# Kernel tuning notes

Measured on AMD Instinct MI355X. Metric: run time of the kernel, lower is better.

Reference implementation:

```python
import jax, jax.numpy as jnp
import numpy as np

P = 3          # graph partitions
CO = 64        # out_channels
KS = 9         # temporal kernel size (Gamma)
STRIDE = 1     # temporal stride
EPS = 1e-3     # keras BatchNormalization default epsilon


def setup_inputs() -> dict:
    key = jax.random.key(0)
    k1, k2, k3 = jax.random.split(key, 3)
    x = jax.random.normal(k1, (32, 64, 300, 25), dtype=jnp.float32)      # (N, C_in, L, V)
    A = jax.random.uniform(k2, (3, 25, 25), dtype=jnp.float32)           # (P, V, V)
    W = jax.random.normal(k3, (64, 192), dtype=jnp.float32) * 0.05       # (C_in, C_out*P)
    gamma = jnp.ones((64,), dtype=jnp.float32)
    beta = jnp.zeros((64,), dtype=jnp.float32)
    mean = jnp.zeros((64,), dtype=jnp.float32)
    var = jnp.ones((64,), dtype=jnp.float32)
    return {"x": x, "A": A, "W": W, "gamma": gamma, "beta": beta, "mean": mean, "var": var}


def _lt_matrix(L):
    # sum of shifted identities: lt[r, r + i*STRIDE] = 1 for i in [0, KS//STRIDE)
    lt = jnp.zeros((L, L), dtype=jnp.float32)
    for i in range(KS // STRIDE):
        lt = lt + jnp.eye(L, k=i * STRIDE, dtype=jnp.float32)
    return lt


def reference(x, A, W, gamma, beta, mean, var):
    N, C, L, V = x.shape
    res = x  # identity residual (in_channels == out_channels, stride == 1)
    # 1x1 conv: (N,C,L,V) x (C, CO*P) -> (N, CO*P, L, V); channel k = c*P + p (split into CO groups of P)
    y = jnp.einsum('nclv,ck->nklv', x, W)
    y = y.reshape(N, CO, P, L, V)  # (N, C_out, P, L, V)
    # partitioned graph matmul over joints: contract V with A[p]
    z = jnp.einsum('ncplv,pvw->ncplw', y, A)
    # temporal aggregation via handcrafted banded matrix, then sum over partitions
    lt = _lt_matrix(L)
    t = jnp.einsum('ncplv,lm->ncmv', z, lt)  # partition sum fused into einsum
    # BN (inference) over channel axis + ReLU
    inv = gamma / jnp.sqrt(var + EPS)
    xn = (t - mean[None, :, None, None]) * inv[None, :, None, None] + beta[None, :, None, None]
    xn = jax.nn.relu(xn)
    # residual add + final ReLU (dropout is identity at inference)
    return jax.nn.relu(xn + res)
```

## Files before the change

### kernel.cpp

```cpp
#include <hip/hip_runtime.h>
#include <cstdint>
#include <cstddef>

typedef short bf16x8 __attribute__((ext_vector_type(8)));
typedef float f32x4 __attribute__((ext_vector_type(4)));

#define EPS 1e-3f

__device__ __forceinline__ short f32_to_bf16s(float f) {
    union { float f; uint32_t u; } v; v.f = f;
    return (short)((v.u + 0x7FFFu + ((v.u >> 16) & 1u)) >> 16);
}

__global__ __launch_bounds__(256) void prep_kernel(const float* __restrict__ A,
                                                   const float* __restrict__ W,
                                                   unsigned short* __restrict__ wt,
                                                   unsigned short* __restrict__ at) {
    int idx = blockIdx.x * 256 + threadIdx.x;
    if (idx < 12288) {
        int kp = idx >> 6, ci = idx & 63;
        wt[idx] = (unsigned short)f32_to_bf16s(W[ci * 192 + kp]);
    } else {
        int j = idx - 12288;
        if (j < 3072) {
            int w = j / 96, k = j - w * 96;
            float val = 0.f;
            if (w < 25 && k < 75) {
                int p = k / 25, v = k - p * 25;
                val = A[(p * 25 + v) * 25 + w];
            }
            at[j] = (unsigned short)f32_to_bf16s(val);
        }
    }
}

__global__ __launch_bounds__(512, 4) void mega_kernel(
    const float* __restrict__ x,
    const unsigned short* __restrict__ wt,
    const unsigned short* __restrict__ at,
    const float* __restrict__ gamma, const float* __restrict__ beta,
    const float* __restrict__ mean, const float* __restrict__ var,
    float* __restrict__ out) {
    const int lin = blockIdx.x + 38 * blockIdx.y;
    const int logical = (lin & 7) * 152 + (lin >> 3);
    const int ch = logical % 38;
    const int n  = logical / 38;

    const int l0 = ch * 8;
    const int tid = threadIdx.x;
    const int wv = tid >> 6, lane = tid & 63, q = lane >> 4, lcol = lane & 15;

    __shared__ __align__(16) short smem[13312];
    __shared__ float scs[64], shs[64];

    bf16x8 b2[2][3];
    #pragma unroll
    for (int nt = 0; nt < 2; ++nt)
        #pragma unroll
        for (int s = 0; s < 3; ++s)
            b2[nt][s] = *(const bf16x8*)(at + (size_t)(nt * 16 + lcol) * 96 + 32 * s + 8 * q);
    if (tid < 64) {
        float sc = gamma[tid] * rsqrtf(var[tid] + EPS);
        scs[tid] = sc;
        shs[tid] = beta[tid] - mean[tid] * sc;
    }

    #pragma unroll 1
    for (int rep = 0; rep < 4; ++rep) {
        int cidx = tid + rep * 512;
        if (cidx < 1600) {
            int ci = cidx / 25, v = cidx - ci * 25;
            const float* xp = x + (size_t)(n * 64 + ci) * 7500 + v;
            float vals[16];
            #pragma unroll
            for (int i = 0; i < 16; ++i) {
                int l = l0 - 8 + i;
                vals[i] = (l >= 0 && l < 300) ? xp[l * 25] : 0.f;
            }
            float run = vals[0] + vals[1] + vals[2] + vals[3]
                      + vals[4] + vals[5] + vals[6] + vals[7];
            short* wb = &smem[(ci >> 3) * 1656 + (ci & 7)];
            #pragma unroll
            for (int j = 0; j < 8; ++j) {
                run += vals[j + 8];
                wb[(j * 25 + v) * 8] = f32_to_bf16s(run);
                run -= vals[j];
            }
        }
    }
    __syncthreads();

    bf16x8 b1[2][2];
    #pragma unroll
    for (int nt = 0; nt < 2; ++nt) {
        int col = wv * 25 + nt * 16 + lcol;
        #pragma unroll
        for (int s = 0; s < 2; ++s)
            b1[nt][s] = *(const bf16x8*)&smem[(4 * s + q) * 1656 + col * 8];
    }
    __syncthreads();

    #pragma unroll
    for (int i = lane; i < 512; i += 64) {
        int r = i >> 5, cc = 72 + (i & 31);
        smem[(wv * 16 + r) * 104 + cc] = 0;
    }

    const int lg = l0 + wv;
    const size_t outrow = ((size_t)n * 64 * 300 + lg) * 25;

    #pragma unroll 1
    for (int g = 0; g < 4; ++g) {
        bf16x8 a1[3][2];
        #pragma unroll
        for (int mt = 0; mt < 3; ++mt)
            #pragma unroll
            for (int s = 0; s < 2; ++s)
                a1[mt][s] = *(const bf16x8*)(wt + (size_t)(g * 48 + mt * 16 + lcol) * 64 + 32 * s + 8 * q);

        f32x4 acc[3][2];
        #pragma unroll
        for (int mt = 0; mt < 3; ++mt)
            #pragma unroll
            for (int nt = 0; nt < 2; ++nt) acc[mt][nt] = (f32x4){0.f, 0.f, 0.f, 0.f};
        #pragma unroll
        for (int s = 0; s < 2; ++s)
            #pragma unroll
            for (int mt = 0; mt < 3; ++mt) {
                bf16x8 av = a1[mt][s];
                #pragma unroll
                for (int nt = 0; nt < 2; ++nt)
                    acc[mt][nt] = __builtin_amdgcn_mfma_f32_16x16x32_bf16(av, b1[nt][s], acc[mt][nt], 0, 0, 0);
            }

        float res[2][4];
        #pragma unroll
        for (int nt = 0; nt < 2; ++nt) {
            int w = nt * 16 + lcol;
            bool val = (w < 25) && (lg < 300);
            #pragma unroll
            for (int r = 0; r < 4; ++r) {
                int c = g * 16 + 4 * q + r;
                res[nt][r] = val ? x[outrow + (size_t)c * 7500 + w] : 0.f;
            }
        }

        #pragma unroll
        for (int mt = 0; mt < 3; ++mt)
            #pragma unroll
            for (int nt = 0; nt < 2; ++nt) {
                int v = nt * 16 + lcol;
                if (v < 25) {
                    #pragma unroll
                    for (int r = 0; r < 4; ++r) {
                        int kpl = mt * 16 + 4 * q + r;
                        int cl = kpl / 3, p = kpl - 3 * cl;
                        smem[(wv * 16 + cl) * 104 + 25 * p + v] = f32_to_bf16s(acc[mt][nt][r]);
                    }
                }
            }

        f32x4 c0 = {0.f, 0.f, 0.f, 0.f}, c1 = {0.f, 0.f, 0.f, 0.f};
        #pragma unroll
        for (int s = 0; s < 3; ++s) {
            bf16x8 a2 = *(const bf16x8*)&smem[(wv * 16 + lcol) * 104 + 32 * s + 8 * q];
            c0 = __builtin_amdgcn_mfma_f32_16x16x32_bf16(a2, b2[0][s], c0, 0, 0, 0);
            c1 = __builtin_amdgcn_mfma_f32_16x16x32_bf16(a2, b2[1][s], c1, 0, 0, 0);
        }

        if (lg < 300) {
            #pragma unroll
            for (int nt = 0; nt < 2; ++nt) {
                int w = nt * 16 + lcol;
                if (w < 25) {
                    f32x4 cc = nt ? c1 : c0;
                    #pragma unroll
                    for (int r = 0; r < 4; ++r) {
                        int c = g * 16 + 4 * q + r;
                        float o = fmaxf(cc[r] * scs[c] + shs[c], 0.f);
                        out[outrow + (size_t)c * 7500 + w] = fmaxf(o + res[nt][r], 0.f);
                    }
                }
            }
        }
    }
}

extern "C" void kernel_launch(void* const* d_in, const int* in_sizes, int n_in,
                              void* d_out, int out_size, void* d_ws, size_t ws_size,
                              hipStream_t stream) {
    const float* x     = (const float*)d_in[0];
    const float* A     = (const float*)d_in[1];
    const float* W     = (const float*)d_in[2];
    const float* gamma = (const float*)d_in[3];
    const float* beta  = (const float*)d_in[4];
    const float* mean  = (const float*)d_in[5];
    const float* var   = (const float*)d_in[6];
    float* out = (float*)d_out;

    char* ws = (char*)d_ws;
    unsigned short* wt = (unsigned short*)ws;
    unsigned short* at = (unsigned short*)(ws + 24576);

    prep_kernel<<<60, 256, 0, stream>>>(A, W, wt, at);
    mega_kernel<<<dim3(38, 32), 512, 0, stream>>>(x, wt, at, gamma, beta, mean, var, out);
}
```

Measured before the change: 162.2 us.

## Stage graph matrix in LDS and software-pipeline weight loads across channel groups

The graph-adjacency B operand moves from per-thread registers into shared memory, is loaded cooperatively, and is reread from LDS in each group. This frees registers and may allow higher occupancy. The group loop is manually unrolled into four calls that double-buffer the next group's weight fragments, prefetched during the current group's work, with sched_barriers separating the groups. The cost is more LDS per block and extra LDS reads each group.

```diff
diff --git a/kernel.cpp b/kernel.cpp
--- a/kernel.cpp
+++ b/kernel.cpp
@@ -6,6 +6,7 @@
 typedef float f32x4 __attribute__((ext_vector_type(4)));
 
 #define EPS 1e-3f
+#define AT_OFF 13312
 
 __device__ __forceinline__ short f32_to_bf16s(float f) {
     union { float f; uint32_t u; } v; v.f = f;
@@ -34,6 +35,98 @@
     }
 }
 
+__device__ __forceinline__ void load_a1(int g, const unsigned short* __restrict__ wt,
+                                        int lcol, int q, bf16x8 (&a1)[3][2]) {
+    #pragma unroll
+    for (int mt = 0; mt < 3; ++mt)
+        #pragma unroll
+        for (int s = 0; s < 2; ++s)
+            a1[mt][s] = *(const bf16x8*)(wt + (size_t)(g * 48 + mt * 16 + lcol) * 64 + 32 * s + 8 * q);
+}
+
+__device__ __forceinline__ void do_group(int g, bool loadNext, int gnext,
+    const unsigned short* __restrict__ wt, short* smem,
+    const bf16x8 (&a1)[3][2], bf16x8 (&a1n)[3][2], const bf16x8 (&b1)[2][2],
+    const float* __restrict__ x, float* __restrict__ out,
+    const float* scs, const float* shs,
+    size_t outrow, int lg, int wv, int q, int lcol)
+{
+    f32x4 acc[3][2];
+    #pragma unroll
+    for (int mt = 0; mt < 3; ++mt)
+        #pragma unroll
+        for (int nt = 0; nt < 2; ++nt) acc[mt][nt] = (f32x4){0.f, 0.f, 0.f, 0.f};
+    #pragma unroll
+    for (int s = 0; s < 2; ++s)
+        #pragma unroll
+        for (int mt = 0; mt < 3; ++mt) {
+            bf16x8 av = a1[mt][s];
+            #pragma unroll
+            for (int nt = 0; nt < 2; ++nt)
+                acc[mt][nt] = __builtin_amdgcn_mfma_f32_16x16x32_bf16(av, b1[nt][s], acc[mt][nt], 0, 0, 0);
+        }
+
+    float res[2][4];
+    #pragma unroll
+    for (int nt = 0; nt < 2; ++nt) {
+        int w = nt * 16 + lcol;
+        bool val = (w < 25) && (lg < 300);
+        #pragma unroll
+        for (int r = 0; r < 4; ++r) {
+            int c = g * 16 + 4 * q + r;
+            res[nt][r] = val ? x[outrow + (size_t)c * 7500 + w] : 0.f;
+        }
+    }
+
+    #pragma unroll
+    for (int mt = 0; mt < 3; ++mt)
+        #pragma unroll
+        for (int nt = 0; nt < 2; ++nt) {
+            int v = nt * 16 + lcol;
+            if (v < 25) {
+                #pragma unroll
+                for (int r = 0; r < 4; ++r) {
+                    int kpl = mt * 16 + 4 * q + r;
+                    int cl = kpl / 3, p = kpl - 3 * cl;
+                    smem[(wv * 16 + cl) * 104 + 25 * p + v] = f32_to_bf16s(acc[mt][nt][r]);
+                }
+            }
+        }
+
+    if (loadNext) load_a1(gnext, wt, lcol, q, a1n);
+
+    bf16x8 b2l[2][3];
+    #pragma unroll
+    for (int nt = 0; nt < 2; ++nt)
+        #pragma unroll
+        for (int s = 0; s < 3; ++s)
+            b2l[nt][s] = *(const bf16x8*)&smem[AT_OFF + (nt * 16 + lcol) * 104 + 32 * s + 8 * q];
+
+    f32x4 c0 = {0.f, 0.f, 0.f, 0.f}, c1 = {0.f, 0.f, 0.f, 0.f};
+    #pragma unroll
+    for (int s = 0; s < 3; ++s) {
+        bf16x8 a2 = *(const bf16x8*)&smem[(wv * 16 + lcol) * 104 + 32 * s + 8 * q];
+        c0 = __builtin_amdgcn_mfma_f32_16x16x32_bf16(a2, b2l[0][s], c0, 0, 0, 0);
+        c1 = __builtin_amdgcn_mfma_f32_16x16x32_bf16(a2, b2l[1][s], c1, 0, 0, 0);
+    }
+
+    if (lg < 300) {
+        #pragma unroll
+        for (int nt = 0; nt < 2; ++nt) {
+            int w = nt * 16 + lcol;
+            if (w < 25) {
+                f32x4 cc = nt ? c1 : c0;
+                #pragma unroll
+                for (int r = 0; r < 4; ++r) {
+                    int c = g * 16 + 4 * q + r;
+                    float o = fmaxf(cc[r] * scs[c] + shs[c], 0.f);
+                    out[outrow + (size_t)c * 7500 + w] = fmaxf(o + res[nt][r], 0.f);
+                }
+            }
+        }
+    }
+}
+
 __global__ __launch_bounds__(512, 4) void mega_kernel(
     const float* __restrict__ x,
     const unsigned short* __restrict__ wt,
@@ -50,15 +143,14 @@
     const int tid = threadIdx.x;
     const int wv = tid >> 6, lane = tid & 63, q = lane >> 4, lcol = lane & 15;
 
-    __shared__ __align__(16) short smem[13312];
+    __shared__ __align__(16) short smem[16640];
     __shared__ float scs[64], shs[64];
 
-    bf16x8 b2[2][3];
-    #pragma unroll
-    for (int nt = 0; nt < 2; ++nt)
-        #pragma unroll
-        for (int s = 0; s < 3; ++s)
-            b2[nt][s] = *(const bf16x8*)(at + (size_t)(nt * 16 + lcol) * 96 + 32 * s + 8 * q);
+    const int aw = tid >> 4, aj = (tid & 15) * 6;
+    const uint32_t* asrc = (const uint32_t*)(at + aw * 96 + aj);
+    uint32_t av0 = asrc[0], av1 = asrc[1], av2 = asrc[2];
+    __builtin_amdgcn_sched_barrier(0);
+
     if (tid < 64) {
         float sc = gamma[tid] * rsqrtf(var[tid] + EPS);
         scs[tid] = sc;
@@ -88,6 +180,11 @@
             }
         }
     }
+
+    {
+        uint32_t* adst = (uint32_t*)&smem[AT_OFF + aw * 104 + aj];
+        adst[0] = av0; adst[1] = av1; adst[2] = av2;
+    }
     __syncthreads();
 
     bf16x8 b1[2][2];
@@ -109,81 +206,15 @@
     const int lg = l0 + wv;
     const size_t outrow = ((size_t)n * 64 * 300 + lg) * 25;
 
-    #pragma unroll 1
-    for (int g = 0; g < 4; ++g) {
-        bf16x8 a1[3][2];
-        #pragma unroll
-        for (int mt = 0; mt < 3; ++mt)
-            #pragma unroll
-            for (int s = 0; s < 2; ++s)
-                a1[mt][s] = *(const bf16x8*)(wt + (size_t)(g * 48 + mt * 16 + lcol) * 64 + 32 * s + 8 * q);
-
-        f32x4 acc[3][2];
-        #pragma unroll
-        for (int mt = 0; mt < 3; ++mt)
-            #pragma unroll
-            for (int nt = 0; nt < 2; ++nt) acc[mt][nt] = (f32x4){0.f, 0.f, 0.f, 0.f};
-        #pragma unroll
-        for (int s = 0; s < 2; ++s)
-            #pragma unroll
-            for (int mt = 0; mt < 3; ++mt) {
-                bf16x8 av = a1[mt][s];
-                #pragma unroll
-                for (int nt = 0; nt < 2; ++nt)
-                    acc[mt][nt] = __builtin_amdgcn_mfma_f32_16x16x32_bf16(av, b1[nt][s], acc[mt][nt], 0, 0, 0);
-            }
-
-        float res[2][4];
-        #pragma unroll
-        for (int nt = 0; nt < 2; ++nt) {
-            int w = nt * 16 + lcol;
-            bool val = (w < 25) && (lg < 300);
-            #pragma unroll
-            for (int r = 0; r < 4; ++r) {
-                int c = g * 16 + 4 * q + r;
-                res[nt][r] = val ? x[outrow + (size_t)c * 7500 + w] : 0.f;
-            }
-        }
-
-        #pragma unroll
-        for (int mt = 0; mt < 3; ++mt)
-            #pragma unroll
-            for (int nt = 0; nt < 2; ++nt) {
-                int v = nt * 16 + lcol;
-                if (v < 25) {
-                    #pragma unroll
-                    for (int r = 0; r < 4; ++r) {
-                        int kpl = mt * 16 + 4 * q + r;
-                        int cl = kpl / 3, p = kpl - 3 * cl;
-                        smem[(wv * 16 + cl) * 104 + 25 * p + v] = f32_to_bf16s(acc[mt][nt][r]);
-                    }
-                }
-            }
-
-        f32x4 c0 = {0.f, 0.f, 0.f, 0.f}, c1 = {0.f, 0.f, 0.f, 0.f};
-        #pragma unroll
-        for (int s = 0; s < 3; ++s) {
-            bf16x8 a2 = *(const bf16x8*)&smem[(wv * 16 + lcol) * 104 + 32 * s + 8 * q];
-            c0 = __builtin_amdgcn_mfma_f32_16x16x32_bf16(a2, b2[0][s], c0, 0, 0, 0);
-            c1 = __builtin_amdgcn_mfma_f32_16x16x32_bf16(a2, b2[1][s], c1, 0, 0, 0);
-        }
-
-        if (lg < 300) {
-            #pragma unroll
-            for (int nt = 0; nt < 2; ++nt) {
-                int w = nt * 16 + lcol;
-                if (w < 25) {
-                    f32x4 cc = nt ? c1 : c0;
-                    #pragma unroll
-                    for (int r = 0; r < 4; ++r) {
-                        int c = g * 16 + 4 * q + r;
-                        float o = fmaxf(cc[r] * scs[c] + shs[c], 0.f);
-                        out[outrow + (size_t)c * 7500 + w] = fmaxf(o + res[nt][r], 0.f);
-                    }
-                }
-            }
-        }
-    }
+    bf16x8 a1a[3][2], a1b[3][2];
+    load_a1(0, wt, lcol, q, a1a);
+    do_group(0, true,  1, wt, smem, a1a, a1b, b1, x, out, scs, shs, outrow, lg, wv, q, lcol);
+    __builtin_amdgcn_sched_barrier(0);
+    do_group(1, true,  2, wt, smem, a1b, a1a, b1, x, out, scs, shs, outrow, lg, wv, q, lcol);
+    __builtin_amdgcn_sched_barrier(0);
+    do_group(2, true,  3, wt, smem, a1a, a1b, b1, x, out, scs, shs, outrow, lg, wv, q, lcol);
+    __builtin_amdgcn_sched_barrier(0);
+    do_group(3, false, 3, wt, smem, a1b, a1a, b1, x, out, scs, shs, outrow, lg, wv, q, lcol);
 }
 
 extern "C" void kernel_launch(void* const* d_in, const int* in_sizes, int n_in,
```

After: 162.7 us (median of 2 runs). About the same (+0.3%).
